# Kernel tuning notes

Hardware: AMD Instinct MI355X
Metric: run time of the kernel (lower is better)

The kernel has to match this reference:

```python
import jax, jax.numpy as jnp
import numpy as np
import math

NUM_ITER = 5
FEAT_STRIDE = 16
GAUSS_SIGMA = 1.0
HINGE_THRESHOLD = -999.0
MIN_FILTER_REG = 1e-3
ALPHA_EPS = 0.0


def apply_filter(feat, weights):
    # feat: (ni, ns, C, H, W); weights: (ns, C, fH, fW) -> scores (ni, ns, oH, oW)
    ni, ns, C, H, W = feat.shape
    fH, fW = weights.shape[-2], weights.shape[-1]
    x = feat.reshape(ni, ns * C, H, W)
    out = jax.lax.conv_general_dilated(
        x, weights, window_strides=(1, 1),
        padding=((fH // 2, fH // 2), (fW // 2, fW // 2)),
        dimension_numbers=('NCHW', 'OIHW', 'NCHW'),
        feature_group_count=ns)
    return out  # (ni, ns, oH, oW); oH = H + (fH+1)%2


def get_label(center, out_sz, sigma):
    # center: (ni, ns, 2) in (row, col) order
    k0 = jnp.arange(out_sz[0], dtype=jnp.float32)[None, None, :, None]
    k1 = jnp.arange(out_sz[1], dtype=jnp.float32)[None, None, None, :]
    g0 = jnp.exp(-0.5 / (sigma * sigma) * (k0 - center[..., 0][..., None, None]) ** 2)
    g1 = jnp.exp(-0.5 / (sigma * sigma) * (k1 - center[..., 1][..., None, None]) ** 2)
    return g0 * g1  # (ni, ns, oH, oW)


def _forward(weights, feat, bb, log_step_length, filter_reg):
    ni, ns = feat.shape[0], feat.shape[1]
    fH, fW = weights.shape[-2], weights.shape[-1]
    out_sz = (feat.shape[-2] + (fH + 1) % 2, feat.shape[-1] + (fW + 1) % 2)
    step = jnp.exp(log_step_length)[0]
    reg = jnp.maximum(filter_reg * filter_reg, MIN_FILTER_REG ** 2)[0]
    dmap_offset = jnp.array([fH % 2, fW % 2], jnp.float32) / 2.0
    # (x, y) -> (row, col), feature-grid coordinates
    center = ((bb[..., :2] + bb[..., 2:] / 2.0) / FEAT_STRIDE)[..., ::-1] - dmap_offset
    label = get_label(center, out_sz, GAUSS_SIGMA)
    mask = (label > HINGE_THRESHOLD).astype(feat.dtype)
    label = label * mask
    sw = math.sqrt(1.0 / ni)

    losses = []
    for _ in range(NUM_ITER):
        scores = apply_filter(feat, weights)
        scores_act = mask * scores + (1.0 - mask) * jax.nn.relu(scores)
        score_mask = mask + (1.0 - mask) * (jax.lax.stop_gradient(scores) > 0).astype(scores.dtype)
        residuals = sw * (scores_act - label)
        losses.append((jnp.sum(residuals ** 2) + reg * jnp.sum(weights ** 2)) / ns)
        residuals_mapped = score_mask * (sw * residuals)
        # feat-transpose = adjoint of apply_filter w.r.t. the filter weights
        _, vjp_fn = jax.vjp(lambda w: apply_filter(feat, w), weights)
        data_grad = vjp_fn(residuals_mapped)[0]
        weights_grad = data_grad + reg * weights
        scores_grad = apply_filter(feat, weights_grad)
        scores_grad = sw * (score_mask * scores_grad)
        alpha_num = jnp.sum(weights_grad ** 2, axis=(1, 2, 3))  # (ns,)
        alpha_den = jnp.maximum(
            jnp.sum(scores_grad.reshape(ni, ns, -1) ** 2, axis=(0, 2))
            + (reg + ALPHA_EPS) * alpha_num, 1e-8)
        alpha = alpha_num / alpha_den
        weights = weights - step * alpha[:, None, None, None] * weights_grad

    scores = apply_filter(feat, weights)
    scores = mask * scores + (1.0 - mask) * jax.nn.relu(scores)
    losses.append((jnp.sum((sw * (scores - label)) ** 2) + reg * jnp.sum(weights ** 2)) / ns)
    return weights, jnp.stack(losses)


def setup_inputs() -> dict:
    key = jax.random.key(0)
    k1, k2, k3, k4 = jax.random.split(key, 4)
    ni, ns, C, H, W, fH, fW = 3, 32, 512, 22, 22, 4, 4
    weights = 0.01 * jax.random.normal(k1, (ns, C, fH, fW), jnp.float32)
    feat = jax.random.normal(k2, (ni, ns, C, H, W), jnp.float32)
    # boxes (x, y, w, h) in image coords (image size = 22*16 = 352)
    xy = jax.random.uniform(k3, (ni, ns, 2), jnp.float32, 50.0, 250.0)
    wh = jax.random.uniform(k4, (ni, ns, 2), jnp.float32, 32.0, 96.0)
    bb = jnp.concatenate([xy, wh], axis=-1)
    log_step_length = jnp.zeros((1,), jnp.float32)  # log(1.0)
    filter_reg = 0.01 * jnp.ones((1,), jnp.float32)
    return {"weights": weights, "feat": feat, "bb": bb,
            "log_step_length": log_step_length, "filter_reg": filter_reg}


def reference(weights, feat, bb, log_step_length, filter_reg):
    return _forward(weights, feat, bb, log_step_length, filter_reg)
```

## Files before the change

### kernel.cpp

```cpp
#include <hip/hip_runtime.h>
#include <hip/hip_fp16.h>

#define NI 3
#define NS 32
#define CHN 512
#define OH 23
#define P2 529
#define NP 50784
#define UV 484
#define WSZ 262144
#define KTOT 1536
#define NKB 48
#define RSP 1544

typedef unsigned int uint32;
typedef unsigned short u16;
typedef _Float16 h2 __attribute__((ext_vector_type(2)));
typedef _Float16 f16x8 __attribute__((ext_vector_type(8)));
typedef float f32x4 __attribute__((ext_vector_type(4)));

#define OFF_FEATT 0UL
#define OFF_LABEL 47579136UL
#define OFF_S0    47782272UL
#define OFF_S1    47985408UL
#define OFF_SGRAW 48188544UL
#define OFF_WG    48391680UL
#define OFF_WGF16 49440256UL
#define OFF_W0F16 49964544UL
#define OFF_PART  50488832UL
#define OFF_FEATC 50521600UL
#define OFF_S0B   100853248UL
#define OFF_SGB   101056384UL

#define P_DEN   0
#define P_NUM   4320
#define P_LOSS  5600
#define P_WSQ0  5760
#define P_WSQA  5792
#define P_WSQ5  6816
#define P_L5    7840

__device__ __forceinline__ float waveSum(float v) {
#pragma unroll
  for (int o = 32; o > 0; o >>= 1) v += __shfl_xor(v, o, 64);
  return v;
}

__global__ __launch_bounds__(256) void k_setup(const float* __restrict__ feat,
                                               const float* __restrict__ w0,
                                               const float* __restrict__ bb,
                                               u16* __restrict__ featT,
                                               u16* __restrict__ w0f16,
                                               float* __restrict__ wmaster,
                                               float* __restrict__ label,
                                               float* __restrict__ part) {
  __shared__ uint32 lds32[64 * 121];
  __shared__ float sred[4];
  int b = blockIdx.x, tid = threadIdx.x;
  if (b < 1536) {
    int snT = b >> 4, r4 = b & 15;
    int cb = r4 >> 1, uvh = r4 & 1;
    int s = snT / 3, n = snT % 3;
    const float* fsrc =
        feat + ((size_t)n * NS + s) * CHN * UV + (size_t)(cb * 64) * UV + uvh * 242;
#pragma unroll
    for (int it = 0; it < 31; ++it) {
      int idx = it * 256 + tid;
      if (idx < 7744) {
        int r = (unsigned)idx / 121u;
        int j = idx - r * 121;
        float2 v = *(const float2*)(fsrc + (size_t)r * UV + 2 * j);
        lds32[idx] = (uint32)__half_as_ushort(__float2half(v.x)) |
                     ((uint32)__half_as_ushort(__float2half(v.y)) << 16);
      }
    }
    __syncthreads();
    uint32* dstT = (uint32*)featT +
                   ((size_t)(snT * 4 + (cb >> 1)) * UV + uvh * 242) * 64 + (cb & 1) * 32;
#pragma unroll
    for (int it = 0; it < 16; ++it) {
      int o = it * 256 + tid;
      if (o < 3872) {
        int uv = o >> 4, kp = o & 15;
        int j = uv >> 1, sh = (uv & 1) * 16;
        uint32 a0 = lds32[(4 * kp + 0) * 121 + j];
        uint32 a1 = lds32[(4 * kp + 1) * 121 + j];
        uint32 a2 = lds32[(4 * kp + 2) * 121 + j];
        uint32 a3 = lds32[(4 * kp + 3) * 121 + j];
        uint2 val;
        val.x = ((a0 >> sh) & 0xffffu) | (((a1 >> sh) & 0xffffu) << 16);
        val.y = ((a2 >> sh) & 0xffffu) | (((a3 >> sh) & 0xffffu) << 16);
        *(uint2*)(dstT + (size_t)uv * 64 + 2 * kp) = val;
      }
    }
  } else if (b < 1568) {
    int s = b - 1536;
    for (int i = tid; i < 8192; i += 256) {
      int tap = i >> 9, c = i & 511;
      w0f16[(size_t)s * 8192 + i] =
          __half_as_ushort(__float2half(w0[(size_t)s * 8192 + c * 16 + tap]));
    }
    float sq = 0.f;
    for (int i = tid; i < 8192; i += 256) {
      float v = w0[(size_t)s * 8192 + i];
      wmaster[(size_t)s * 8192 + i] = v;
      sq += v * v;
    }
    sq = waveSum(sq);
    if ((tid & 63) == 0) sred[tid >> 6] = sq;
    __syncthreads();
    if (tid == 0) part[P_WSQ0 + s] = sred[0] + sred[1] + sred[2] + sred[3];
  } else {
    int p = (b - 1568) * 256 + tid;
    if (p < NP) {
      int nsid = p / P2, rem = p % P2;
      int i = rem / OH, j = rem % OH;
      const float* bp = bb + (size_t)nsid * 4;
      float cr = (bp[1] + 0.5f * bp[3]) * 0.0625f;
      float cc = (bp[0] + 0.5f * bp[2]) * 0.0625f;
      float dy = (float)i - cr, dx = (float)j - cc;
      label[p] = __expf(-0.5f * (dy * dy + dx * dx));
    }
  }
}

__global__ __launch_bounds__(1024) void k_conv_fwd(const u16* __restrict__ featT,
                                                   const u16* __restrict__ wf16,
                                                   float* __restrict__ outA,
                                                   float* __restrict__ outB) {
  __shared__ uint32 w_lds[16 * 132];
  __shared__ float G[496 * 17];
  int tid = threadIdx.x;
  int bidx = blockIdx.x;
  int snT = bidx >> 1, ch = bidx & 1;
  int s = snT / 3, n = snT - s * 3;
  const uint32* wsrc = (const uint32*)(wf16 + (size_t)s * 8192) + ch * 128;
  for (int i = tid; i < 2048; i += 1024) {
    int tap = i >> 7, p = i & 127;
    w_lds[tap * 132 + p] = wsrc[(size_t)tap * 256 + p];
  }
  __syncthreads();
  int wave = tid >> 6, lane = tid & 63;
  int q = lane >> 4, m16 = lane & 15;
  int t0 = wave, t1 = wave + 16;
  bool has2 = (t1 < 31);
  f32x4 acc0 = {0.f, 0.f, 0.f, 0.f}, acc1 = {0.f, 0.f, 0.f, 0.f};
  size_t base = (size_t)snT * 4 * UV * 128;
  int r0i = t0 * 16 + m16;
  int r1i = has2 ? t1 * 16 + m16 : 483;
  if (r1i > 483) r1i = 483;
  size_t row0 = (size_t)r0i * 128;
  size_t row1 = (size_t)r1i * 128;
#pragma unroll
  for (int ks = 0; ks < 8; ++ks) {
    int cb = ch * 2 + (ks >> 2), cin = (ks & 3) * 32;
    size_t cbase = base + (size_t)cb * UV * 128 + cin + q * 8;
    f16x8 a0 = *(const f16x8*)(featT + cbase + row0);
    uint4 bw = *(const uint4*)&w_lds[m16 * 132 + ks * 16 + q * 4];
    f16x8 bf = __builtin_bit_cast(f16x8, bw);
    acc0 = __builtin_amdgcn_mfma_f32_16x16x32_f16(a0, bf, acc0, 0, 0, 0);
    if (has2) {
      f16x8 a1 = *(const f16x8*)(featT + cbase + row1);
      acc1 = __builtin_amdgcn_mfma_f32_16x16x32_f16(a1, bf, acc1, 0, 0, 0);
    }
  }
#pragma unroll
  for (int r = 0; r < 4; ++r) G[(t0 * 16 + q * 4 + r) * 17 + m16] = acc0[r];
  if (has2) {
#pragma unroll
    for (int r = 0; r < 4; ++r) G[(t1 * 16 + q * 4 + r) * 17 + m16] = acc1[r];
  }
  __syncthreads();
  if (tid < P2) {
    int y = tid / 23, x = tid - y * 23;
    float val = 0.f;
#pragma unroll
    for (int ky = 0; ky < 4; ++ky) {
      int u = y + ky - 2;
      if ((unsigned)u < 22u) {
#pragma unroll
        for (int kx = 0; kx < 4; ++kx) {
          int v = x + kx - 2;
          if ((unsigned)v < 22u) val += G[(u * 22 + v) * 17 + ky * 4 + kx];
        }
      }
    }
    float* dst = ch ? outB : outA;
    dst[(size_t)(n * NS + s) * P2 + tid] = val;
  }
}

__global__ __launch_bounds__(1024) void k_adjoint(
    int t, const float* __restrict__ feat, u16* __restrict__ featC,
    const float* __restrict__ label, const float* __restrict__ s0a,
    const float* __restrict__ s0b, const float* __restrict__ scores_old,
    float* __restrict__ scores_new, const float* __restrict__ sga,
    const float* __restrict__ sgb, float* __restrict__ wg, u16* __restrict__ wgf16,
    float* __restrict__ wmaster, float* __restrict__ part, const float* __restrict__ lsl,
    const float* __restrict__ fr) {
  __shared__ float r_lds[3 * P2];
  __shared__ float g_lds[1587];
  __shared__ __align__(16) u16 rs[16 * RSP];
  __shared__ __align__(16) float kred[3 * 4 * 64 * 4];
  __shared__ float lred[16], nred[16], wred[16], dend[16];
  int tid = threadIdx.x;
  int s = blockIdx.x >> 3, chunk = blockIdx.x & 7;
  int c0 = chunk * 64;
  float step = __expf(lsl[0]);
  float frv = fr[0];
  float reg = fmaxf(frv * frv, 1e-6f);

  float alpha_p = 0.f;
  if (t >= 1) {
    const float* np_ = part + P_NUM + (size_t)((t - 1) * NS + s) * 8;
    float nu = 0.f;
#pragma unroll
    for (int i = 0; i < 8; ++i) nu += np_[i];
    float dp = 0.f;
    for (int pl = tid; pl < 1587; pl += 1024) {
      int nn = (unsigned)pl / (unsigned)P2;
      int rem = pl - nn * P2;
      size_t gp = (size_t)(nn * NS + s) * P2 + rem;
      float g = sga[gp] + sgb[gp];
      g_lds[pl] = g;
      dp += g * g;
    }
    dp = waveSum(dp);
    if ((tid & 63) == 0) dend[tid >> 6] = dp;
    __syncthreads();
    float de = 0.f;
#pragma unroll
    for (int i = 0; i < 16; ++i) de += dend[i];
    alpha_p = nu / fmaxf(de * (1.0f / 3.0f) + reg * nu, 1e-8f);
  }

  float lsum = 0.f;
  for (int pl = tid; pl < 1587; pl += 1024) {
    int nn = (unsigned)pl / (unsigned)P2;
    int rem = pl - nn * P2;
    size_t gp = (size_t)(nn * NS + s) * P2 + rem;
    float S = (t <= 1) ? (s0a[gp] + s0b[gp]) : scores_old[gp];
    if (t >= 1) S -= step * alpha_p * g_lds[pl];
    float d = S - label[gp];
    r_lds[nn * P2 + rem] = d * (1.0f / 3.0f);
    if (chunk == 0) {
      if (t >= 1) scores_new[gp] = S;
      lsum += d * d;
    }
  }
  lsum = waveSum(lsum);
  if ((tid & 63) == 0) lred[tid >> 6] = lsum;
  __syncthreads();
  if (chunk == 0 && tid == 0) {
    float L = 0.f;
#pragma unroll
    for (int i = 0; i < 16; ++i) L += lred[i];
    part[P_LOSS + t * NS + s] = L * (1.0f / 3.0f);
  }

  for (int idx = tid; idx < 16 * RSP; idx += 1024) {
    int tap = (unsigned)idx / (unsigned)RSP;
    int k = idx - tap * RSP;
    float val = 0.f;
    if (k < KTOT) {
      int n = k >> 9, uv = k & 511;
      if (uv < UV) {
        int u = (unsigned)uv / 22u;
        int v = uv - u * 22;
        int ky = tap >> 2, kx = tap & 3;
        int y = u + 2 - ky, x = v + 2 - kx;
        if ((unsigned)y < 23u && (unsigned)x < 23u) val = r_lds[n * P2 + y * OH + x];
      }
    }
    rs[idx] = __half_as_ushort(__float2half(val));
  }
  __syncthreads();

  int wave = tid >> 6, lane = tid & 63;
  int q = lane >> 4, m16 = lane & 15;
  int tile = wave & 3, kq = wave >> 2;
  int c = c0 + tile * 16 + m16;
  const u16* brow = rs + m16 * RSP + kq * 384 + q * 8;
  f32x4 acc = {0.f, 0.f, 0.f, 0.f};
  if (t == 0) {
#pragma unroll
    for (int ks = 0; ks < 12; ++ks) {
      int kb = kq * 12 + ks;
      int k0 = kb * 32 + q * 8;
      int nn = k0 >> 9, uv0 = k0 & 511;
      float v[8];
#pragma unroll
      for (int i = 0; i < 8; ++i) v[i] = 0.f;
      if (uv0 < UV) {
        const float* fsrc = feat + ((size_t)(nn * NS + s) * CHN + c) * UV + uv0;
        if (uv0 + 8 <= UV) {
          float4 p0 = *(const float4*)fsrc;
          float4 p1 = *(const float4*)(fsrc + 4);
          v[0] = p0.x; v[1] = p0.y; v[2] = p0.z; v[3] = p0.w;
          v[4] = p1.x; v[5] = p1.y; v[6] = p1.z; v[7] = p1.w;
        } else {
#pragma unroll
          for (int i = 0; i < 4; ++i) v[i] = fsrc[i];
        }
      }
      union { u16 h[8]; f16x8 f; uint4 u; } av;
#pragma unroll
      for (int i = 0; i < 8; ++i) av.h[i] = __half_as_ushort(__float2half(v[i]));
      *(uint4*)(featC + (((size_t)(s * NKB + kb) * CHN + c) * 32 + q * 8)) = av.u;
      f16x8 bf = *(const f16x8*)(brow + ks * 32);
      acc = __builtin_amdgcn_mfma_f32_16x16x32_f16(av.f, bf, acc, 0, 0, 0);
    }
  } else {
    const u16* arow = featC + ((size_t)(s * NKB + kq * 12) * CHN + c) * 32 + q * 8;
#pragma unroll
    for (int ks = 0; ks < 12; ++ks) {
      f16x8 a = *(const f16x8*)(arow + (size_t)ks * (CHN * 32));
      f16x8 bf = *(const f16x8*)(brow + ks * 32);
      acc = __builtin_amdgcn_mfma_f32_16x16x32_f16(a, bf, acc, 0, 0, 0);
    }
  }
  if (kq) *(f32x4*)&kred[(((kq - 1) * 4 + tile) * 64 + lane) * 4] = acc;
  __syncthreads();

  float num_part = 0.f, wsq_part = 0.f;
  if (kq == 0) {
#pragma unroll
    for (int kk = 0; kk < 3; ++kk)
      acc += *(const f32x4*)&kred[((kk * 4 + tile) * 64 + lane) * 4];
    int tap = m16;
    int ccb = c0 + tile * 16 + q * 4;
    union { u16 h[4]; uint2 v2; } pk;
#pragma unroll
    for (int r = 0; r < 4; ++r) {
      int cc = ccb + r;
      size_t widx = (size_t)s * 8192 + (size_t)cc * 16 + tap;
      float wold = wmaster[widx];
      float wnew = wold;
      if (t >= 1) {
        wnew = wold - step * alpha_p * wg[widx];
        wmaster[widx] = wnew;
      }
      float wgn = acc[r] + reg * wnew;
      wg[widx] = wgn;
      pk.h[r] = __half_as_ushort(__float2half(wgn));
      wsq_part += wnew * wnew;
      num_part += wgn * wgn;
    }
    *(uint2*)&wgf16[(size_t)s * 8192 + (size_t)tap * 512 + ccb] = pk.v2;
  }
  num_part = waveSum(num_part);
  wsq_part = waveSum(wsq_part);
  if (lane == 0) {
    nred[wave] = num_part;
    wred[wave] = wsq_part;
  }
  __syncthreads();
  if (tid == 0) {
    float nsum = 0.f, wsum = 0.f;
#pragma unroll
    for (int i = 0; i < 16; ++i) {
      nsum += nred[i];
      wsum += wred[i];
    }
    part[P_NUM + (size_t)(t * NS + s) * 8 + chunk] = nsum;
    if (t >= 1) part[P_WSQA + (size_t)((t - 1) * NS + s) * 8 + chunk] = wsum;
  }
}

__global__ __launch_bounds__(1024) void k_den(const float* __restrict__ sga,
                                              const float* __restrict__ sgb,
                                              float* __restrict__ part) {
  __shared__ float dend[16];
  int s = blockIdx.x, tid = threadIdx.x;
  float dp = 0.f;
  for (int pl = tid; pl < 1587; pl += 1024) {
    int nn = (unsigned)pl / (unsigned)P2;
    int rem = pl - nn * P2;
    size_t gp = (size_t)(nn * NS + s) * P2 + rem;
    float g = sga[gp] + sgb[gp];
    dp += g * g;
  }
  dp = waveSum(dp);
  if ((tid & 63) == 0) dend[tid >> 6] = dp;
  __syncthreads();
  if (tid == 0) {
    float de = 0.f;
#pragma unroll
    for (int i = 0; i < 16; ++i) de += dend[i];
    part[P_DEN + s] = de * (1.0f / 3.0f);
  }
}

__device__ __forceinline__ float alphaFinal(const float* __restrict__ part, int s,
                                            float reg) {
  const float* np_ = part + P_NUM + (size_t)(4 * NS + s) * 8;
  float nu = 0.f;
#pragma unroll
  for (int i = 0; i < 8; ++i) nu += np_[i];
  float de = part[P_DEN + s];
  return nu / fmaxf(de + reg * nu, 1e-8f);
}

__global__ void k_final(float* __restrict__ wmaster, const float* __restrict__ wg,
                        const float* __restrict__ scores4, const float* __restrict__ sga,
                        const float* __restrict__ sgb, const float* __restrict__ label,
                        float* __restrict__ part, const float* __restrict__ lsl,
                        const float* __restrict__ fr) {
  __shared__ float alpha_s[32];
  __shared__ float red4[4];
  int b = blockIdx.x, tid = threadIdx.x;
  float step = __expf(lsl[0]);
  float frv = fr[0];
  float reg = fmaxf(frv * frv, 1e-6f);
  if (tid < 32) alpha_s[tid] = alphaFinal(part, tid, reg);
  __syncthreads();
  if (b < 1024) {
    int idx = b * 256 + tid;
    int s = idx >> 13;
    float w5 = wmaster[idx] - step * alpha_s[s] * wg[idx];
    wmaster[idx] = w5;
    float sq = waveSum(w5 * w5);
    if ((tid & 63) == 0) red4[tid >> 6] = sq;
    __syncthreads();
    if (tid == 0) part[P_WSQ5 + b] = red4[0] + red4[1] + red4[2] + red4[3];
  } else {
    int p = (b - 1024) * 256 + tid;
    float contrib = 0.f;
    if (p < NP) {
      int nsid = p / P2;
      int s = nsid & 31;
      float s5 = scores4[p] - step * alpha_s[s] * (sga[p] + sgb[p]);
      float d = s5 - label[p];
      contrib = d * d;
    }
    contrib = waveSum(contrib);
    if ((tid & 63) == 0) red4[tid >> 6] = contrib;
    __syncthreads();
    if (tid == 0)
      part[P_L5 + (b - 1024)] = (red4[0] + red4[1] + red4[2] + red4[3]) * (1.0f / 3.0f);
  }
}

__global__ void k_losses(float* __restrict__ out_losses, const float* __restrict__ part,
                         const float* __restrict__ fr) {
  __shared__ float red[8];
  int tid = threadIdx.x;
  float frv = fr[0];
  float reg = fmaxf(frv * frv, 1e-6f);
  float v5 = 0.f;
  for (int i = tid; i < 1024; i += 256) v5 += part[P_WSQ5 + i];
  v5 = waveSum(v5);
  if ((tid & 63) == 0) red[tid >> 6] = v5;
  __syncthreads();
  float wsq5 = red[0] + red[1] + red[2] + red[3];
  float l5 = 0.f;
  for (int i = tid; i < 199; i += 256) l5 += part[P_L5 + i];
  l5 = waveSum(l5);
  if ((tid & 63) == 0) red[4 + (tid >> 6)] = l5;
  __syncthreads();
  float loss5 = red[4] + red[5] + red[6] + red[7];
  if (tid < 5) {
    int t = tid;
    float ls = 0.f;
    for (int i = 0; i < 32; ++i) ls += part[P_LOSS + t * NS + i];
    float ws_ = 0.f;
    if (t == 0) {
      for (int i = 0; i < 32; ++i) ws_ += part[P_WSQ0 + i];
    } else {
      for (int i = 0; i < 256; ++i) ws_ += part[P_WSQA + (t - 1) * 256 + i];
    }
    out_losses[t] = (ls + reg * ws_) * (1.0f / 32.0f);
  }
  if (tid == 5) out_losses[5] = (loss5 + reg * wsq5) * (1.0f / 32.0f);
}

extern "C" void kernel_launch(void* const* d_in, const int* in_sizes, int n_in,
                              void* d_out, int out_size, void* d_ws, size_t ws_size,
                              hipStream_t stream) {
  const float* w0 = (const float*)d_in[0];
  const float* feat = (const float*)d_in[1];
  const float* bb = (const float*)d_in[2];
  const float* lsl = (const float*)d_in[3];
  const float* fr = (const float*)d_in[4];
  float* out = (float*)d_out;
  char* ws = (char*)d_ws;
  u16* featT = (u16*)(ws + OFF_FEATT);
  float* label = (float*)(ws + OFF_LABEL);
  float* s0 = (float*)(ws + OFF_S0);
  float* s0b = (float*)(ws + OFF_S0B);
  float* s1 = (float*)(ws + OFF_S1);
  float* sga = (float*)(ws + OFF_SGRAW);
  float* sgb = (float*)(ws + OFF_SGB);
  float* wg = (float*)(ws + OFF_WG);
  u16* wgf16 = (u16*)(ws + OFF_WGF16);
  u16* w0f16 = (u16*)(ws + OFF_W0F16);
  float* part = (float*)(ws + OFF_PART);
  u16* featC = (u16*)(ws + OFF_FEATC);

  k_setup<<<1767, 256, 0, stream>>>(feat, w0, bb, featT, w0f16, out, label, part);
  k_conv_fwd<<<192, 1024, 0, stream>>>(featT, w0f16, s0, s0b);
  for (int t = 0; t < 5; ++t) {
    const float* so = (t <= 1) ? s0 : ((t & 1) ? s0 : s1);
    float* sn = (t & 1) ? s1 : s0;
    k_adjoint<<<256, 1024, 0, stream>>>(t, feat, featC, label, s0, s0b, so, sn, sga, sgb,
                                        wg, wgf16, out, part, lsl, fr);
    k_conv_fwd<<<192, 1024, 0, stream>>>(featT, wgf16, sga, sgb);
  }
  k_den<<<32, 1024, 0, stream>>>(sga, sgb, part);
  k_final<<<1223, 256, 0, stream>>>(out, wg, s0, sga, sgb, label, part, lsl, fr);
  k_losses<<<1, 256, 0, stream>>>(out + WSZ, part, fr);
}
```

Before: 360.1 us.

## Fuse forward conv of gradient into adjoint kernel with per-chunk partial outputs

The k_conv_fwd launch that applied the gradient filter is removed each iteration. Each adjoint block now stages its 64-channel slice of the new fp16 gradient in shared memory, runs MFMA against featT for its channel chunk, and writes per-chunk partial score maps into an 8-way partial buffer. Consumers (next adjoint, k_den, k_final) sum the 8 partials. This saves five launches and the wgf16 global round trip, at the cost of more shared-memory use and extra partial-sum reads.

```diff
diff --git a/kernel.cpp b/kernel.cpp
--- a/kernel.cpp
+++ b/kernel.cpp
@@ -23,14 +23,13 @@
 #define OFF_LABEL 47579136UL
 #define OFF_S0    47782272UL
 #define OFF_S1    47985408UL
-#define OFF_SGRAW 48188544UL
 #define OFF_WG    48391680UL
 #define OFF_WGF16 49440256UL
 #define OFF_W0F16 49964544UL
 #define OFF_PART  50488832UL
 #define OFF_FEATC 50521600UL
 #define OFF_S0B   100853248UL
-#define OFF_SGB   101056384UL
+#define OFF_SGP   101259520UL
 
 #define P_DEN   0
 #define P_NUM   4320
@@ -191,17 +190,21 @@
 }
 
 __global__ __launch_bounds__(1024) void k_adjoint(
-    int t, const float* __restrict__ feat, u16* __restrict__ featC,
-    const float* __restrict__ label, const float* __restrict__ s0a,
-    const float* __restrict__ s0b, const float* __restrict__ scores_old,
-    float* __restrict__ scores_new, const float* __restrict__ sga,
-    const float* __restrict__ sgb, float* __restrict__ wg, u16* __restrict__ wgf16,
-    float* __restrict__ wmaster, float* __restrict__ part, const float* __restrict__ lsl,
+    int t, const float* __restrict__ feat, const u16* __restrict__ featT,
+    u16* __restrict__ featC, const float* __restrict__ label,
+    const float* __restrict__ s0a, const float* __restrict__ s0b,
+    const float* __restrict__ scores_old, float* __restrict__ scores_new,
+    float* __restrict__ sgp, float* __restrict__ wg, float* __restrict__ wmaster,
+    float* __restrict__ part, const float* __restrict__ lsl,
     const float* __restrict__ fr) {
   __shared__ float r_lds[3 * P2];
   __shared__ float g_lds[1587];
-  __shared__ __align__(16) u16 rs[16 * RSP];
+  __shared__ __align__(16) union ShPool {
+    u16 rs[16 * RSP];
+    float G[496 * 17];
+  } shp;
   __shared__ __align__(16) float kred[3 * 4 * 64 * 4];
+  __shared__ __align__(8) u16 wgB[16 * 72];
   __shared__ float lred[16], nred[16], wred[16], dend[16];
   int tid = threadIdx.x;
   int s = blockIdx.x >> 3, chunk = blockIdx.x & 7;
@@ -221,7 +224,9 @@
       int nn = (unsigned)pl / (unsigned)P2;
       int rem = pl - nn * P2;
       size_t gp = (size_t)(nn * NS + s) * P2 + rem;
-      float g = sga[gp] + sgb[gp];
+      float g = 0.f;
+#pragma unroll
+      for (int ch = 0; ch < 8; ++ch) g += sgp[(size_t)ch * NP + gp];
       g_lds[pl] = g;
       dp += g * g;
     }
@@ -272,7 +277,7 @@
         if ((unsigned)y < 23u && (unsigned)x < 23u) val = r_lds[n * P2 + y * OH + x];
       }
     }
-    rs[idx] = __half_as_ushort(__float2half(val));
+    shp.rs[idx] = __half_as_ushort(__float2half(val));
   }
   __syncthreads();
 
@@ -280,7 +285,7 @@
   int q = lane >> 4, m16 = lane & 15;
   int tile = wave & 3, kq = wave >> 2;
   int c = c0 + tile * 16 + m16;
-  const u16* brow = rs + m16 * RSP + kq * 384 + q * 8;
+  const u16* brow = shp.rs + m16 * RSP + kq * 384 + q * 8;
   f32x4 acc = {0.f, 0.f, 0.f, 0.f};
   if (t == 0) {
 #pragma unroll
@@ -346,7 +351,7 @@
       wsq_part += wnew * wnew;
       num_part += wgn * wgn;
     }
-    *(uint2*)&wgf16[(size_t)s * 8192 + (size_t)tap * 512 + ccb] = pk.v2;
+    *(uint2*)&wgB[m16 * 72 + tile * 16 + q * 4] = pk.v2;
   }
   num_part = waveSum(num_part);
   wsq_part = waveSum(wsq_part);
@@ -365,10 +370,59 @@
     part[P_NUM + (size_t)(t * NS + s) * 8 + chunk] = nsum;
     if (t >= 1) part[P_WSQA + (size_t)((t - 1) * NS + s) * 8 + chunk] = wsum;
   }
-}
-
-__global__ __launch_bounds__(1024) void k_den(const float* __restrict__ sga,
-                                              const float* __restrict__ sgb,
+  __syncthreads();
+
+  f16x8 bf0 = *(const f16x8*)&wgB[m16 * 72 + q * 8];
+  f16x8 bf1 = *(const f16x8*)&wgB[m16 * 72 + 32 + q * 8];
+  int cbb = chunk >> 1;
+  int chalf = (chunk & 1) * 64;
+  for (int n = 0; n < 3; ++n) {
+    int snT = s * 3 + n;
+    const u16* ab = featT + (size_t)(snT * 4 + cbb) * UV * 128 + chalf + q * 8;
+    {
+      int r0 = wave * 16 + m16;
+      const u16* ap = ab + (size_t)r0 * 128;
+      f32x4 a0 = {0.f, 0.f, 0.f, 0.f};
+      a0 = __builtin_amdgcn_mfma_f32_16x16x32_f16(*(const f16x8*)ap, bf0, a0, 0, 0, 0);
+      a0 = __builtin_amdgcn_mfma_f32_16x16x32_f16(*(const f16x8*)(ap + 32), bf1, a0, 0,
+                                                  0, 0);
+#pragma unroll
+      for (int r = 0; r < 4; ++r) shp.G[(wave * 16 + q * 4 + r) * 17 + m16] = a0[r];
+      if (wave < 15) {
+        int r1 = (wave + 16) * 16 + m16;
+        if (r1 > 483) r1 = 483;
+        const u16* ap1 = ab + (size_t)r1 * 128;
+        f32x4 a1 = {0.f, 0.f, 0.f, 0.f};
+        a1 = __builtin_amdgcn_mfma_f32_16x16x32_f16(*(const f16x8*)ap1, bf0, a1, 0, 0, 0);
+        a1 = __builtin_amdgcn_mfma_f32_16x16x32_f16(*(const f16x8*)(ap1 + 32), bf1, a1,
+                                                    0, 0, 0);
+#pragma unroll
+        for (int r = 0; r < 4; ++r)
+          shp.G[((wave + 16) * 16 + q * 4 + r) * 17 + m16] = a1[r];
+      }
+    }
+    __syncthreads();
+    if (tid < P2) {
+      int y = tid / 23, x = tid - y * 23;
+      float val = 0.f;
+#pragma unroll
+      for (int ky = 0; ky < 4; ++ky) {
+        int u = y + ky - 2;
+        if ((unsigned)u < 22u) {
+#pragma unroll
+          for (int kx = 0; kx < 4; ++kx) {
+            int v = x + kx - 2;
+            if ((unsigned)v < 22u) val += shp.G[(u * 22 + v) * 17 + ky * 4 + kx];
+          }
+        }
+      }
+      sgp[(size_t)chunk * NP + (size_t)(n * NS + s) * P2 + tid] = val;
+    }
+    __syncthreads();
+  }
+}
+
+__global__ __launch_bounds__(1024) void k_den(const float* __restrict__ sgp,
                                               float* __restrict__ part) {
   __shared__ float dend[16];
   int s = blockIdx.x, tid = threadIdx.x;
@@ -377,7 +431,9 @@
     int nn = (unsigned)pl / (unsigned)P2;
     int rem = pl - nn * P2;
     size_t gp = (size_t)(nn * NS + s) * P2 + rem;
-    float g = sga[gp] + sgb[gp];
+    float g = 0.f;
+#pragma unroll
+    for (int ch = 0; ch < 8; ++ch) g += sgp[(size_t)ch * NP + gp];
     dp += g * g;
   }
   dp = waveSum(dp);
@@ -402,10 +458,9 @@
 }
 
 __global__ void k_final(float* __restrict__ wmaster, const float* __restrict__ wg,
-                        const float* __restrict__ scores4, const float* __restrict__ sga,
-                        const float* __restrict__ sgb, const float* __restrict__ label,
-                        float* __restrict__ part, const float* __restrict__ lsl,
-                        const float* __restrict__ fr) {
+                        const float* __restrict__ scores4, const float* __restrict__ sgp,
+                        const float* __restrict__ label, float* __restrict__ part,
+                        const float* __restrict__ lsl, const float* __restrict__ fr) {
   __shared__ float alpha_s[32];
   __shared__ float red4[4];
   int b = blockIdx.x, tid = threadIdx.x;
@@ -429,7 +484,10 @@
     if (p < NP) {
       int nsid = p / P2;
       int s = nsid & 31;
-      float s5 = scores4[p] - step * alpha_s[s] * (sga[p] + sgb[p]);
+      float g = 0.f;
+#pragma unroll
+      for (int ch = 0; ch < 8; ++ch) g += sgp[(size_t)ch * NP + p];
+      float s5 = scores4[p] - step * alpha_s[s] * g;
       float d = s5 - label[p];
       contrib = d * d;
     }
@@ -489,10 +547,8 @@
   float* s0 = (float*)(ws + OFF_S0);
   float* s0b = (float*)(ws + OFF_S0B);
   float* s1 = (float*)(ws + OFF_S1);
-  float* sga = (float*)(ws + OFF_SGRAW);
-  float* sgb = (float*)(ws + OFF_SGB);
+  float* sgp = (float*)(ws + OFF_SGP);
   float* wg = (float*)(ws + OFF_WG);
-  u16* wgf16 = (u16*)(ws + OFF_WGF16);
   u16* w0f16 = (u16*)(ws + OFF_W0F16);
   float* part = (float*)(ws + OFF_PART);
   u16* featC = (u16*)(ws + OFF_FEATC);
@@ -502,11 +558,10 @@
   for (int t = 0; t < 5; ++t) {
     const float* so = (t <= 1) ? s0 : ((t & 1) ? s0 : s1);
     float* sn = (t & 1) ? s1 : s0;
-    k_adjoint<<<256, 1024, 0, stream>>>(t, feat, featC, label, s0, s0b, so, sn, sga, sgb,
-                                        wg, wgf16, out, part, lsl, fr);
-    k_conv_fwd<<<192, 1024, 0, stream>>>(featT, wgf16, sga, sgb);
-  }
-  k_den<<<32, 1024, 0, stream>>>(sga, sgb, part);
-  k_final<<<1223, 256, 0, stream>>>(out, wg, s0, sga, sgb, label, part, lsl, fr);
+    k_adjoint<<<256, 1024, 0, stream>>>(t, feat, featT, featC, label, s0, s0b, so, sn,
+                                        sgp, wg, out, part, lsl, fr);
+  }
+  k_den<<<32, 1024, 0, stream>>>(sgp, part);
+  k_final<<<1223, 256, 0, stream>>>(out, wg, s0, sgp, label, part, lsl, fr);
   k_losses<<<1, 256, 0, stream>>>(out + WSZ, part, fr);
 }
```

Result: faster. 345.6 us (-4.0%).
